# Performance work log

Hardware: AMD Instinct MI355X
Metric: run time of the kernel (lower is better)

The kernel has to match this reference:

```python
import jax, jax.numpy as jnp
import numpy as np

B, N, D = 4096, 64, 128
H, ATT = 8, 32
SCALE = ATT ** -0.5


def setup_inputs() -> dict:
    key = jax.random.key(0)
    k1, k2, k3, k4, k5 = jax.random.split(key, 5)
    x = jax.random.normal(k1, (B, N, D), dtype=jnp.float32)
    # glorot-ish scale for weights
    W_Q = jax.random.normal(k2, (H, D, ATT), dtype=jnp.float32) * (2.0 / (D + ATT)) ** 0.5
    W_K = jax.random.normal(k3, (H, D, ATT), dtype=jnp.float32) * (2.0 / (D + ATT)) ** 0.5
    W_V = jax.random.normal(k4, (H, D, ATT), dtype=jnp.float32) * (2.0 / (D + ATT)) ** 0.5
    W_res = jax.random.normal(k5, (D, H * ATT), dtype=jnp.float32) * (2.0 / (D + H * ATT)) ** 0.5
    return {"x": x, "W_Q": W_Q, "W_K": W_K, "W_V": W_V, "W_res": W_res}


def reference(x, W_Q, W_K, W_V, W_res):
    # per-head projections: (B,N,D) x (H,D,K) -> (B,H,N,K)
    Q = jnp.einsum('bnd,hdk->bhnk', x, W_Q)
    K = jnp.einsum('bnd,hdk->bhnk', x, W_K)
    V = jnp.einsum('bnd,hdk->bhnk', x, W_V)
    scores = jnp.einsum('bhnk,bhmk->bhnm', Q, K) * SCALE  # (B,H,N,N)
    attn = jax.nn.softmax(scores, axis=-1)
    ctx = jnp.einsum('bhnm,bhmk->bhnk', attn, V)          # (B,H,N,K)
    ctx = ctx.transpose(0, 2, 1, 3).reshape(x.shape[0], x.shape[1], H * ATT)
    res = x @ W_res  # d != H*att_dim -> residual projection
    return jax.nn.relu(ctx + res)
```

## Files before the change

kernel.cpp:

```cpp
#include <hip/hip_runtime.h>

#define NB    4096
#define SEQ   64
#define DIM   128
#define NHEAD 8
#define ATTD  32
#define HKC   256
#define SCALE 0.17677669529663687f
#define LOG2E 1.4426950408889634f

typedef __bf16 bf16_t;
typedef __bf16 bf16x8 __attribute__((ext_vector_type(8)));
typedef __bf16 bf16x4 __attribute__((ext_vector_type(4)));
typedef float  f32x4  __attribute__((ext_vector_type(4)));
typedef unsigned int u32;

static __device__ __forceinline__ u32 pkbf(float a, float b) {
  unsigned short ua = __builtin_bit_cast(unsigned short, (__bf16)a);
  unsigned short ub = __builtin_bit_cast(unsigned short, (__bf16)b);
  return (u32)ua | ((u32)ub << 16);
}

static __device__ __forceinline__ bf16x8 merge2(f32x4 t0, f32x4 t1, int lo, int g) {
  u32 p0 = pkbf(t0[0], t0[1]);
  u32 p1 = pkbf(t0[2], t0[3]);
  u32 q0 = pkbf(t1[0], t1[1]);
  u32 q1 = pkbf(t1[2], t1[3]);
  const int srcA = lo + ((g & 1) << 5);
  const int srcB = srcA + 16;
  u32 a0 = (u32)__shfl((int)p0, srcA, 64);
  u32 a1 = (u32)__shfl((int)p1, srcA, 64);
  u32 b0 = (u32)__shfl((int)p0, srcB, 64);
  u32 b1 = (u32)__shfl((int)p1, srcB, 64);
  u32 c0 = (u32)__shfl((int)q0, srcA, 64);
  u32 c1 = (u32)__shfl((int)q1, srcA, 64);
  u32 d0 = (u32)__shfl((int)q0, srcB, 64);
  u32 d1 = (u32)__shfl((int)q1, srcB, 64);
  const bool glow = (g < 2);
  union { u32 u[4]; bf16x8 v; } r;
  r.u[0] = glow ? a0 : c0;
  r.u[1] = glow ? a1 : c1;
  r.u[2] = glow ? b0 : d0;
  r.u[3] = glow ? b1 : d1;
  return r.v;
}

#define XSWZ(r, c) (((r) << 7) + ((c) ^ (((r) & 7) << 3)))
#define VSWZ(r, c) (((r) << 6) + ((c) ^ (((r) & 7) << 3)))
#define PSWZ(r, c) (((r) << 6) + ((c) ^ (((r) & 7) << 3)))

__global__ void prep_weights(const float* __restrict__ Wq,
                             const float* __restrict__ Wk,
                             const float* __restrict__ Wv,
                             const float* __restrict__ Wr,
                             bf16_t* __restrict__ ws) {
  int idx = blockIdx.x * 256 + threadIdx.x;
  int m = idx >> 15;
  int e = idx & 32767;
  int c = e >> 7;
  int d = e & 127;
  float v;
  if (m == 0)      v = Wq[((c >> 5) * DIM + d) * ATTD + (c & 31)] * (SCALE * LOG2E);
  else if (m == 1) v = Wk[((c >> 5) * DIM + d) * ATTD + (c & 31)];
  else if (m == 2) v = Wv[((c >> 5) * DIM + d) * ATTD + (c & 31)];
  else             v = Wr[d * HKC + c];
  ws[idx] = (bf16_t)v;
}

__launch_bounds__(256, 3)
__global__ void fused_attn(const float* __restrict__ xg,
                           const bf16_t* __restrict__ ws,
                           float* __restrict__ outg) {
  __shared__ bf16_t Xb[64 * 128];
  __shared__ bf16_t VP[4][2048];

  const int t  = threadIdx.x;
  const int w  = t >> 6;
  const int l  = t & 63;
  const int lo = l & 15;
  const int g  = l >> 4;
  const int b  = blockIdx.x;

  bf16_t* const vtw = VP[w];
  bf16_t* const ptw = VP[w];

  {
    const float* xb = xg + (size_t)b * (SEQ * DIM);
#pragma unroll
    for (int i = 0; i < 8; ++i) {
      int idx = i * 1024 + t * 4;
      float4 v = *(const float4*)(xb + idx);
      bf16x4 p;
      p[0] = (bf16_t)v.x; p[1] = (bf16_t)v.y; p[2] = (bf16_t)v.z; p[3] = (bf16_t)v.w;
      *(bf16x4*)&Xb[XSWZ(idx >> 7, idx & 127)] = p;
    }
  }
  __syncthreads();

  const bf16_t* wsq = ws;
  const bf16_t* wsk = ws + 32768;
  const bf16_t* wsv = ws + 65536;
  const bf16_t* wsr = ws + 98304;
  float* ob = outg + (size_t)b * (SEQ * HKC);
  const f32x4 z4 = {0.f, 0.f, 0.f, 0.f};

#pragma unroll
  for (int hh = 0; hh < 2; ++hh) {
    const int hc = w * 64 + hh * 32;

    f32x4 acck[2][4];
#pragma unroll
    for (int i = 0; i < 2; ++i)
#pragma unroll
      for (int j = 0; j < 4; ++j) acck[i][j] = z4;
#pragma unroll
    for (int kk = 0; kk < 4; ++kk) {
      bf16x8 aw[2], bx[4];
#pragma unroll
      for (int at = 0; at < 2; ++at)
        aw[at] = *(const bf16x8*)(wsk + (hc + at * 16 + lo) * DIM + kk * 32 + g * 8);
#pragma unroll
      for (int nt = 0; nt < 4; ++nt)
        bx[nt] = *(const bf16x8*)&Xb[XSWZ(nt * 16 + lo, kk * 32 + g * 8)];
      __builtin_amdgcn_s_setprio(1);
#pragma unroll
      for (int at = 0; at < 2; ++at)
#pragma unroll
        for (int nt = 0; nt < 4; ++nt)
          acck[at][nt] = __builtin_amdgcn_mfma_f32_16x16x32_bf16(aw[at], bx[nt], acck[at][nt], 0, 0, 0);
      __builtin_amdgcn_s_setprio(0);
    }

    f32x4 accv[4][2];
#pragma unroll
    for (int i = 0; i < 4; ++i)
#pragma unroll
      for (int j = 0; j < 2; ++j) accv[i][j] = z4;
#pragma unroll
    for (int kk = 0; kk < 4; ++kk) {
      bf16x8 ax[4], bw[2];
#pragma unroll
      for (int nt = 0; nt < 4; ++nt)
        ax[nt] = *(const bf16x8*)&Xb[XSWZ(nt * 16 + lo, kk * 32 + g * 8)];
#pragma unroll
      for (int ct = 0; ct < 2; ++ct)
        bw[ct] = *(const bf16x8*)(wsv + (hc + ct * 16 + lo) * DIM + kk * 32 + g * 8);
      __builtin_amdgcn_s_setprio(1);
#pragma unroll
      for (int nt = 0; nt < 4; ++nt)
#pragma unroll
        for (int ct = 0; ct < 2; ++ct)
          accv[nt][ct] = __builtin_amdgcn_mfma_f32_16x16x32_bf16(ax[nt], bw[ct], accv[nt][ct], 0, 0, 0);
      __builtin_amdgcn_s_setprio(0);
    }

    bf16x8 kf[4];
#pragma unroll
    for (int nt = 0; nt < 4; ++nt) kf[nt] = merge2(acck[0][nt], acck[1][nt], lo, g);

#pragma unroll
    for (int nt = 0; nt < 4; ++nt)
#pragma unroll
      for (int ct = 0; ct < 2; ++ct) {
        uint2 d;
        d.x = pkbf(accv[nt][ct][0], accv[nt][ct][1]);
        d.y = pkbf(accv[nt][ct][2], accv[nt][ct][3]);
        *(uint2*)&vtw[VSWZ(ct * 16 + lo, nt * 16 + 4 * g)] = d;
      }

    f32x4 accq[2][4];
#pragma unroll
    for (int i = 0; i < 2; ++i)
#pragma unroll
      for (int j = 0; j < 4; ++j) accq[i][j] = z4;
#pragma unroll
    for (int kk = 0; kk < 4; ++kk) {
      bf16x8 aw[2], bx[4];
#pragma unroll
      for (int at = 0; at < 2; ++at)
        aw[at] = *(const bf16x8*)(wsq + (hc + at * 16 + lo) * DIM + kk * 32 + g * 8);
#pragma unroll
      for (int mt = 0; mt < 4; ++mt)
        bx[mt] = *(const bf16x8*)&Xb[XSWZ(mt * 16 + lo, kk * 32 + g * 8)];
      __builtin_amdgcn_s_setprio(1);
#pragma unroll
      for (int at = 0; at < 2; ++at)
#pragma unroll
        for (int mt = 0; mt < 4; ++mt)
          accq[at][mt] = __builtin_amdgcn_mfma_f32_16x16x32_bf16(aw[at], bx[mt], accq[at][mt], 0, 0, 0);
      __builtin_amdgcn_s_setprio(0);
    }

    bf16x8 vf[2][2];
#pragma unroll
    for (int ct = 0; ct < 2; ++ct)
#pragma unroll
      for (int kk2 = 0; kk2 < 2; ++kk2)
        vf[ct][kk2] = *(const bf16x8*)&vtw[VSWZ(ct * 16 + lo, kk2 * 32 + g * 8)];

    bf16x8 qf[4];
#pragma unroll
    for (int mt = 0; mt < 4; ++mt) qf[mt] = merge2(accq[0][mt], accq[1][mt], lo, g);

    f32x4 ch[2][4];
#pragma unroll
    for (int i = 0; i < 2; ++i)
#pragma unroll
      for (int j = 0; j < 4; ++j) ch[i][j] = z4;
#pragma unroll
    for (int mt = 0; mt < 4; ++mt) {
      bf16_t* const pt = ptw + ((mt & 1) << 10);
      f32x4 sv[4];
      __builtin_amdgcn_s_setprio(1);
#pragma unroll
      for (int nt = 0; nt < 4; ++nt)
        sv[nt] = __builtin_amdgcn_mfma_f32_16x16x32_bf16(kf[nt], qf[mt], z4, 0, 0, 0);
      __builtin_amdgcn_s_setprio(0);
      bf16x8 bxr[4], awr[2];
#pragma unroll
      for (int mtj = 0; mtj < 4; ++mtj)
        bxr[mtj] = *(const bf16x8*)&Xb[XSWZ(mtj * 16 + lo, mt * 32 + g * 8)];
#pragma unroll
      for (int ct = 0; ct < 2; ++ct)
        awr[ct] = *(const bf16x8*)(wsr + (hc + ct * 16 + lo) * DIM + mt * 32 + g * 8);
      float ps[4];
#pragma unroll
      for (int nt = 0; nt < 4; ++nt) {
        float e0 = __builtin_amdgcn_exp2f(sv[nt][0]);
        float e1 = __builtin_amdgcn_exp2f(sv[nt][1]);
        float e2 = __builtin_amdgcn_exp2f(sv[nt][2]);
        float e3 = __builtin_amdgcn_exp2f(sv[nt][3]);
        sv[nt][0] = e0; sv[nt][1] = e1; sv[nt][2] = e2; sv[nt][3] = e3;
        ps[nt] = (e0 + e1) + (e2 + e3);
      }
      float sum = (ps[0] + ps[1]) + (ps[2] + ps[3]);
#pragma unroll
      for (int nt = 0; nt < 4; ++nt) {
        uint2 d;
        d.x = pkbf(sv[nt][0], sv[nt][1]);
        d.y = pkbf(sv[nt][2], sv[nt][3]);
        *(uint2*)&pt[PSWZ(lo, nt * 16 + 4 * g)] = d;
      }
      __builtin_amdgcn_s_setprio(1);
#pragma unroll
      for (int ct = 0; ct < 2; ++ct)
#pragma unroll
        for (int mtj = 0; mtj < 4; ++mtj)
          ch[ct][mtj] = __builtin_amdgcn_mfma_f32_16x16x32_bf16(awr[ct], bxr[mtj], ch[ct][mtj], 0, 0, 0);
      __builtin_amdgcn_s_setprio(0);
      sum += __shfl_xor(sum, 16, 64);
      sum += __shfl_xor(sum, 32, 64);
      float rinv = __builtin_amdgcn_rcpf(sum);
      bf16x8 pf0 = *(const bf16x8*)&pt[PSWZ(lo, g * 8)];
      bf16x8 pf1 = *(const bf16x8*)&pt[PSWZ(lo, 32 + g * 8)];
      __builtin_amdgcn_s_setprio(1);
#pragma unroll
      for (int ct = 0; ct < 2; ++ct) {
        f32x4 a = __builtin_amdgcn_mfma_f32_16x16x32_bf16(vf[ct][0], pf0, z4, 0, 0, 0);
        a = __builtin_amdgcn_mfma_f32_16x16x32_bf16(vf[ct][1], pf1, a, 0, 0, 0);
#pragma unroll
        for (int j = 0; j < 4; ++j)
          ch[ct][mt][j] = fmaf(a[j], rinv, ch[ct][mt][j]);
      }
      __builtin_amdgcn_s_setprio(0);
    }

#pragma unroll
    for (int ct = 0; ct < 2; ++ct)
#pragma unroll
      for (int mt = 0; mt < 4; ++mt) {
        float4 o;
        o.x = fmaxf(ch[ct][mt][0], 0.f);
        o.y = fmaxf(ch[ct][mt][1], 0.f);
        o.z = fmaxf(ch[ct][mt][2], 0.f);
        o.w = fmaxf(ch[ct][mt][3], 0.f);
        *(float4*)(ob + (mt * 16 + lo) * HKC + hc + ct * 16 + 4 * g) = o;
      }
  }
}

extern "C" void kernel_launch(void* const* d_in, const int* in_sizes, int n_in,
                              void* d_out, int out_size, void* d_ws, size_t ws_size,
                              hipStream_t stream) {
  const float* x  = (const float*)d_in[0];
  const float* Wq = (const float*)d_in[1];
  const float* Wk = (const float*)d_in[2];
  const float* Wv = (const float*)d_in[3];
  const float* Wr = (const float*)d_in[4];
  bf16_t* ws = (bf16_t*)d_ws;
  float* out = (float*)d_out;

  prep_weights<<<512, 256, 0, stream>>>(Wq, Wk, Wv, Wr, ws);
  fused_attn<<<NB, 256, 0, stream>>>(x, ws, out);
}
```

Measured before the change: 180.8 us.

## Restructure residual accumulation per query tile and raise occupancy to four blocks

The residual projection is now computed per query tile mt, with a full K-loop over D inside each mt iteration. Each output tile is stored right after its attention contribution, so the 8 persistent ch accumulators become 2 short-lived ones. Scoping the K, V and Q projection accumulators also shortens register live ranges. Together these cut register pressure so launch bounds can ask for 4 blocks per SIMD instead of 3, trading more per-tile load/MFMA interleaving for higher occupancy and latency hiding.

```diff
diff --git a/kernel.cpp b/kernel.cpp
--- a/kernel.cpp
+++ b/kernel.cpp
@@ -67,7 +67,7 @@
   ws[idx] = (bf16_t)v;
 }
 
-__launch_bounds__(256, 3)
+__launch_bounds__(256, 4)
 __global__ void fused_attn(const float* __restrict__ xg,
                            const bf16_t* __restrict__ ws,
                            float* __restrict__ outg) {
@@ -108,105 +108,101 @@
   for (int hh = 0; hh < 2; ++hh) {
     const int hc = w * 64 + hh * 32;
 
-    f32x4 acck[2][4];
-#pragma unroll
-    for (int i = 0; i < 2; ++i)
-#pragma unroll
-      for (int j = 0; j < 4; ++j) acck[i][j] = z4;
-#pragma unroll
-    for (int kk = 0; kk < 4; ++kk) {
-      bf16x8 aw[2], bx[4];
-#pragma unroll
-      for (int at = 0; at < 2; ++at)
-        aw[at] = *(const bf16x8*)(wsk + (hc + at * 16 + lo) * DIM + kk * 32 + g * 8);
+    bf16x8 kf[4], vf[2][2], qf[4];
+
+    {
+      f32x4 acck[2][4];
+#pragma unroll
+      for (int i = 0; i < 2; ++i)
+#pragma unroll
+        for (int j = 0; j < 4; ++j) acck[i][j] = z4;
+#pragma unroll
+      for (int kk = 0; kk < 4; ++kk) {
+        bf16x8 aw[2], bx[4];
+#pragma unroll
+        for (int at = 0; at < 2; ++at)
+          aw[at] = *(const bf16x8*)(wsk + (hc + at * 16 + lo) * DIM + kk * 32 + g * 8);
+#pragma unroll
+        for (int nt = 0; nt < 4; ++nt)
+          bx[nt] = *(const bf16x8*)&Xb[XSWZ(nt * 16 + lo, kk * 32 + g * 8)];
+        __builtin_amdgcn_s_setprio(1);
+#pragma unroll
+        for (int at = 0; at < 2; ++at)
+#pragma unroll
+          for (int nt = 0; nt < 4; ++nt)
+            acck[at][nt] = __builtin_amdgcn_mfma_f32_16x16x32_bf16(aw[at], bx[nt], acck[at][nt], 0, 0, 0);
+        __builtin_amdgcn_s_setprio(0);
+      }
+#pragma unroll
+      for (int nt = 0; nt < 4; ++nt) kf[nt] = merge2(acck[0][nt], acck[1][nt], lo, g);
+    }
+
+    {
+      f32x4 accv[4][2];
+#pragma unroll
+      for (int i = 0; i < 4; ++i)
+#pragma unroll
+        for (int j = 0; j < 2; ++j) accv[i][j] = z4;
+#pragma unroll
+      for (int kk = 0; kk < 4; ++kk) {
+        bf16x8 ax[4], bw[2];
+#pragma unroll
+        for (int nt = 0; nt < 4; ++nt)
+          ax[nt] = *(const bf16x8*)&Xb[XSWZ(nt * 16 + lo, kk * 32 + g * 8)];
+#pragma unroll
+        for (int ct = 0; ct < 2; ++ct)
+          bw[ct] = *(const bf16x8*)(wsv + (hc + ct * 16 + lo) * DIM + kk * 32 + g * 8);
+        __builtin_amdgcn_s_setprio(1);
+#pragma unroll
+        for (int nt = 0; nt < 4; ++nt)
+#pragma unroll
+          for (int ct = 0; ct < 2; ++ct)
+            accv[nt][ct] = __builtin_amdgcn_mfma_f32_16x16x32_bf16(ax[nt], bw[ct], accv[nt][ct], 0, 0, 0);
+        __builtin_amdgcn_s_setprio(0);
+      }
 #pragma unroll
       for (int nt = 0; nt < 4; ++nt)
-        bx[nt] = *(const bf16x8*)&Xb[XSWZ(nt * 16 + lo, kk * 32 + g * 8)];
-      __builtin_amdgcn_s_setprio(1);
-#pragma unroll
-      for (int at = 0; at < 2; ++at)
-#pragma unroll
-        for (int nt = 0; nt < 4; ++nt)
-          acck[at][nt] = __builtin_amdgcn_mfma_f32_16x16x32_bf16(aw[at], bx[nt], acck[at][nt], 0, 0, 0);
-      __builtin_amdgcn_s_setprio(0);
-    }
-
-    f32x4 accv[4][2];
-#pragma unroll
-    for (int i = 0; i < 4; ++i)
-#pragma unroll
-      for (int j = 0; j < 2; ++j) accv[i][j] = z4;
-#pragma unroll
-    for (int kk = 0; kk < 4; ++kk) {
-      bf16x8 ax[4], bw[2];
-#pragma unroll
-      for (int nt = 0; nt < 4; ++nt)
-        ax[nt] = *(const bf16x8*)&Xb[XSWZ(nt * 16 + lo, kk * 32 + g * 8)];
+#pragma unroll
+        for (int ct = 0; ct < 2; ++ct) {
+          uint2 d;
+          d.x = pkbf(accv[nt][ct][0], accv[nt][ct][1]);
+          d.y = pkbf(accv[nt][ct][2], accv[nt][ct][3]);
+          *(uint2*)&vtw[VSWZ(ct * 16 + lo, nt * 16 + 4 * g)] = d;
+        }
 #pragma unroll
       for (int ct = 0; ct < 2; ++ct)
-        bw[ct] = *(const bf16x8*)(wsv + (hc + ct * 16 + lo) * DIM + kk * 32 + g * 8);
-      __builtin_amdgcn_s_setprio(1);
-#pragma unroll
-      for (int nt = 0; nt < 4; ++nt)
-#pragma unroll
-        for (int ct = 0; ct < 2; ++ct)
-          accv[nt][ct] = __builtin_amdgcn_mfma_f32_16x16x32_bf16(ax[nt], bw[ct], accv[nt][ct], 0, 0, 0);
-      __builtin_amdgcn_s_setprio(0);
-    }
-
-    bf16x8 kf[4];
-#pragma unroll
-    for (int nt = 0; nt < 4; ++nt) kf[nt] = merge2(acck[0][nt], acck[1][nt], lo, g);
-
-#pragma unroll
-    for (int nt = 0; nt < 4; ++nt)
-#pragma unroll
-      for (int ct = 0; ct < 2; ++ct) {
-        uint2 d;
-        d.x = pkbf(accv[nt][ct][0], accv[nt][ct][1]);
-        d.y = pkbf(accv[nt][ct][2], accv[nt][ct][3]);
-        *(uint2*)&vtw[VSWZ(ct * 16 + lo, nt * 16 + 4 * g)] = d;
-      }
-
-    f32x4 accq[2][4];
-#pragma unroll
-    for (int i = 0; i < 2; ++i)
-#pragma unroll
-      for (int j = 0; j < 4; ++j) accq[i][j] = z4;
-#pragma unroll
-    for (int kk = 0; kk < 4; ++kk) {
-      bf16x8 aw[2], bx[4];
-#pragma unroll
-      for (int at = 0; at < 2; ++at)
-        aw[at] = *(const bf16x8*)(wsq + (hc + at * 16 + lo) * DIM + kk * 32 + g * 8);
-#pragma unroll
-      for (int mt = 0; mt < 4; ++mt)
-        bx[mt] = *(const bf16x8*)&Xb[XSWZ(mt * 16 + lo, kk * 32 + g * 8)];
-      __builtin_amdgcn_s_setprio(1);
-#pragma unroll
-      for (int at = 0; at < 2; ++at)
+#pragma unroll
+        for (int kk2 = 0; kk2 < 2; ++kk2)
+          vf[ct][kk2] = *(const bf16x8*)&vtw[VSWZ(ct * 16 + lo, kk2 * 32 + g * 8)];
+    }
+
+    {
+      f32x4 accq[2][4];
+#pragma unroll
+      for (int i = 0; i < 2; ++i)
+#pragma unroll
+        for (int j = 0; j < 4; ++j) accq[i][j] = z4;
+#pragma unroll
+      for (int kk = 0; kk < 4; ++kk) {
+        bf16x8 aw[2], bx[4];
+#pragma unroll
+        for (int at = 0; at < 2; ++at)
+          aw[at] = *(const bf16x8*)(wsq + (hc + at * 16 + lo) * DIM + kk * 32 + g * 8);
 #pragma unroll
         for (int mt = 0; mt < 4; ++mt)
-          accq[at][mt] = __builtin_amdgcn_mfma_f32_16x16x32_bf16(aw[at], bx[mt], accq[at][mt], 0, 0, 0);
-      __builtin_amdgcn_s_setprio(0);
-    }
-
-    bf16x8 vf[2][2];
-#pragma unroll
-    for (int ct = 0; ct < 2; ++ct)
-#pragma unroll
-      for (int kk2 = 0; kk2 < 2; ++kk2)
-        vf[ct][kk2] = *(const bf16x8*)&vtw[VSWZ(ct * 16 + lo, kk2 * 32 + g * 8)];
-
-    bf16x8 qf[4];
-#pragma unroll
-    for (int mt = 0; mt < 4; ++mt) qf[mt] = merge2(accq[0][mt], accq[1][mt], lo, g);
-
-    f32x4 ch[2][4];
-#pragma unroll
-    for (int i = 0; i < 2; ++i)
-#pragma unroll
-      for (int j = 0; j < 4; ++j) ch[i][j] = z4;
+          bx[mt] = *(const bf16x8*)&Xb[XSWZ(mt * 16 + lo, kk * 32 + g * 8)];
+        __builtin_amdgcn_s_setprio(1);
+#pragma unroll
+        for (int at = 0; at < 2; ++at)
+#pragma unroll
+          for (int mt = 0; mt < 4; ++mt)
+            accq[at][mt] = __builtin_amdgcn_mfma_f32_16x16x32_bf16(aw[at], bx[mt], accq[at][mt], 0, 0, 0);
+        __builtin_amdgcn_s_setprio(0);
+      }
+#pragma unroll
+      for (int mt = 0; mt < 4; ++mt) qf[mt] = merge2(accq[0][mt], accq[1][mt], lo, g);
+    }
+
 #pragma unroll
     for (int mt = 0; mt < 4; ++mt) {
       bf16_t* const pt = ptw + ((mt & 1) << 10);
@@ -216,13 +212,6 @@
       for (int nt = 0; nt < 4; ++nt)
         sv[nt] = __builtin_amdgcn_mfma_f32_16x16x32_bf16(kf[nt], qf[mt], z4, 0, 0, 0);
       __builtin_amdgcn_s_setprio(0);
-      bf16x8 bxr[4], awr[2];
-#pragma unroll
-      for (int mtj = 0; mtj < 4; ++mtj)
-        bxr[mtj] = *(const bf16x8*)&Xb[XSWZ(mtj * 16 + lo, mt * 32 + g * 8)];
-#pragma unroll
-      for (int ct = 0; ct < 2; ++ct)
-        awr[ct] = *(const bf16x8*)(wsr + (hc + ct * 16 + lo) * DIM + mt * 32 + g * 8);
       float ps[4];
 #pragma unroll
       for (int nt = 0; nt < 4; ++nt) {
@@ -241,13 +230,17 @@
         d.y = pkbf(sv[nt][2], sv[nt][3]);
         *(uint2*)&pt[PSWZ(lo, nt * 16 + 4 * g)] = d;
       }
-      __builtin_amdgcn_s_setprio(1);
-#pragma unroll
-      for (int ct = 0; ct < 2; ++ct)
-#pragma unroll
-        for (int mtj = 0; mtj < 4; ++mtj)
-          ch[ct][mtj] = __builtin_amdgcn_mfma_f32_16x16x32_bf16(awr[ct], bxr[mtj], ch[ct][mtj], 0, 0, 0);
-      __builtin_amdgcn_s_setprio(0);
+      f32x4 ch[2] = {z4, z4};
+#pragma unroll
+      for (int kk = 0; kk < 4; ++kk) {
+        bf16x8 bxr = *(const bf16x8*)&Xb[XSWZ(mt * 16 + lo, kk * 32 + g * 8)];
+        bf16x8 awr0 = *(const bf16x8*)(wsr + (hc + lo) * DIM + kk * 32 + g * 8);
+        bf16x8 awr1 = *(const bf16x8*)(wsr + (hc + 16 + lo) * DIM + kk * 32 + g * 8);
+        __builtin_amdgcn_s_setprio(1);
+        ch[0] = __builtin_amdgcn_mfma_f32_16x16x32_bf16(awr0, bxr, ch[0], 0, 0, 0);
+        ch[1] = __builtin_amdgcn_mfma_f32_16x16x32_bf16(awr1, bxr, ch[1], 0, 0, 0);
+        __builtin_amdgcn_s_setprio(0);
+      }
       sum += __shfl_xor(sum, 16, 64);
       sum += __shfl_xor(sum, 32, 64);
       float rinv = __builtin_amdgcn_rcpf(sum);
@@ -260,22 +253,19 @@
         a = __builtin_amdgcn_mfma_f32_16x16x32_bf16(vf[ct][1], pf1, a, 0, 0, 0);
 #pragma unroll
         for (int j = 0; j < 4; ++j)
-          ch[ct][mt][j] = fmaf(a[j], rinv, ch[ct][mt][j]);
+          ch[ct][j] = fmaf(a[j], rinv, ch[ct][j]);
       }
       __builtin_amdgcn_s_setprio(0);
-    }
-
-#pragma unroll
-    for (int ct = 0; ct < 2; ++ct)
-#pragma unroll
-      for (int mt = 0; mt < 4; ++mt) {
+#pragma unroll
+      for (int ct = 0; ct < 2; ++ct) {
         float4 o;
-        o.x = fmaxf(ch[ct][mt][0], 0.f);
-        o.y = fmaxf(ch[ct][mt][1], 0.f);
-        o.z = fmaxf(ch[ct][mt][2], 0.f);
-        o.w = fmaxf(ch[ct][mt][3], 0.f);
+        o.x = fmaxf(ch[ct][0], 0.f);
+        o.y = fmaxf(ch[ct][1], 0.f);
+        o.z = fmaxf(ch[ct][2], 0.f);
+        o.w = fmaxf(ch[ct][3], 0.f);
         *(float4*)(ob + (mt * 16 + lo) * HKC + hc + ct * 16 + 4 * g) = o;
       }
+    }
   }
 }
 
```

Result: slower. 256.0 us (+41.6%).
